# Optimization experiments

Hardware: AMD Instinct MI355X
Metric: run time of the kernel (lower is better)

Reference implementation:

```python
import jax, jax.numpy as jnp
import numpy as np
import math

B, N, K, C = 2, 8192, 16, 64
PE_DIM, HID = 32, 16
SIGMA, EPS = 1.0, 1e-06


def setup_inputs() -> dict:
    key = jax.random.key(0)
    ks = jax.random.split(key, 8)
    p = jax.random.normal(ks[0], (B, N, 3), jnp.float32)
    f = jax.random.normal(ks[1], (B, C, N), jnp.float32)
    pe = jax.random.normal(ks[2], (B, C, N, K), jnp.float32)
    knn_idx = jax.random.randint(ks[3], (B, N, K), 0, N, jnp.int32)
    # LocalAggregation convs1: 1x1 conv [C -> C] (+ReLU)
    W1 = jax.random.normal(ks[4], (C, C), jnp.float32) * (1.0 / math.sqrt(C))
    b1 = jnp.zeros((C,), jnp.float32)
    # GaussianKDEOffsetGenerator params: pe_mlp Linear(3->32), ffn Linear(32->16)->Linear(16->3)
    Wpe = jax.random.normal(ks[5], (PE_DIM, 3), jnp.float32) * (1.0 / math.sqrt(3))
    bpe = jnp.zeros((PE_DIM,), jnp.float32)
    Wh1 = jax.random.normal(ks[6], (HID, PE_DIM), jnp.float32) * (1.0 / math.sqrt(PE_DIM))
    bh1 = jnp.zeros((HID,), jnp.float32)
    Wh2 = jax.random.normal(ks[7], (3, HID), jnp.float32) * (1.0 / math.sqrt(HID))
    bh2 = jnp.zeros((3,), jnp.float32)
    return {"p": p, "f": f, "pe": pe, "W1": W1, "b1": b1, "Wpe": Wpe,
            "bpe": bpe, "Wh1": Wh1, "bh1": bh1, "Wh2": Wh2, "bh2": bh2,
            "knn_idx": knn_idx}


def reference(p, f, pe, W1, b1, Wpe, bpe, Wh1, bh1, Wh2, bh2, knn_idx):
    gather = jax.vmap(lambda a, i: a[i])  # per-batch neighbor gather
    # --- LocalAggregation: convs1 (1x1 conv + relu), group_by_idx, pe+fj, max-pool over K ---
    h = jax.nn.relu(jnp.einsum('oc,bcn->bon', W1, f) + b1[None, :, None])  # [B,C,N]
    ht = jnp.transpose(h, (0, 2, 1))                                       # [B,N,C]
    fj = gather(ht, knn_idx)                                               # [B,N,K,C]
    fout = jnp.max(pe + jnp.transpose(fj, (0, 3, 1, 2)), axis=-1)          # [B,C,N]
    # --- GaussianKDEOffsetGenerator on grouped neighbor coords [B*N, K, 3] ---
    coords = gather(p, knn_idx).reshape(B * N, K, 3)
    rel = coords[:, :, None, :] - coords[:, None, :, :]                    # [BN,K,K,3]
    pek = jax.nn.relu(jnp.einsum('nijc,dc->nijd', rel, Wpe) + bpe).mean(axis=2)  # [BN,K,PE]
    dist2 = jnp.sum(rel * rel, axis=-1)                                    # [BN,K,K]
    coef = 1.0 / math.sqrt(2.0 * math.pi * SIGMA ** 2 + EPS)
    kde = (coef * jnp.exp(-dist2 / (2.0 * SIGMA ** 2 + EPS))).sum(axis=2, keepdims=True)
    kde = kde / (jnp.max(kde, axis=1, keepdims=True) + EPS)                # [BN,K,1]
    fused = pek * kde
    delta = jax.nn.relu(fused @ Wh1.T + bh1) @ Wh2.T + bh2                 # [BN,K,3]
    return (fout, delta)
```

## Files before the change

### kernel.cpp

```cpp
#include <hip/hip_runtime.h>

#define B_ 2
#define N_ 8192
#define K_ 16
#define C_ 64
#define PE_ 32
#define HID_ 16

typedef float f4 __attribute__((ext_vector_type(4)));

__device__ __forceinline__ f4 splat4(float x) { f4 r = {x, x, x, x}; return r; }
__device__ __forceinline__ f4 relu4(f4 v) {
  f4 r;
  r[0] = fmaxf(v[0], 0.f); r[1] = fmaxf(v[1], 0.f);
  r[2] = fmaxf(v[2], 0.f); r[3] = fmaxf(v[3], 0.f);
  return r;
}
__device__ __forceinline__ float dot4(float4 w, f4 v) {
  return fmaf(w.x, v[0], fmaf(w.y, v[1], fmaf(w.z, v[2], w.w * v[3])));
}

struct PK4 { f4 k0, k1, k2, k3; };

__device__ __forceinline__ PK4 channel(const float4* __restrict__ sq,
                                       int d, const float* __restrict__ Wpe,
                                       const float* __restrict__ bpe) {
  const float wx = Wpe[d * 3 + 0], wy = Wpe[d * 3 + 1], wz = Wpe[d * 3 + 2];
  const float wb = bpe[d];
  const float4 A0 = sq[0], B0 = sq[1], C0 = sq[2];
  const float4 A1 = sq[3], B1 = sq[4], C1 = sq[5];
  const float4 A2 = sq[6], B2 = sq[7], C2 = sq[8];
  const float4 A3 = sq[9], B3 = sq[10], C3 = sq[11];
  const float p0  = fmaf(wx, A0.x, fmaf(wy, A0.y, wz * A0.z));
  const float p1  = fmaf(wx, A0.w, fmaf(wy, B0.x, wz * B0.y));
  const float p2  = fmaf(wx, B0.z, fmaf(wy, B0.w, wz * C0.x));
  const float p3  = fmaf(wx, C0.y, fmaf(wy, C0.z, wz * C0.w));
  const float p4  = fmaf(wx, A1.x, fmaf(wy, A1.y, wz * A1.z));
  const float p5  = fmaf(wx, A1.w, fmaf(wy, B1.x, wz * B1.y));
  const float p6  = fmaf(wx, B1.z, fmaf(wy, B1.w, wz * C1.x));
  const float p7  = fmaf(wx, C1.y, fmaf(wy, C1.z, wz * C1.w));
  const float p8  = fmaf(wx, A2.x, fmaf(wy, A2.y, wz * A2.z));
  const float p9  = fmaf(wx, A2.w, fmaf(wy, B2.x, wz * B2.y));
  const float p10 = fmaf(wx, B2.z, fmaf(wy, B2.w, wz * C2.x));
  const float p11 = fmaf(wx, C2.y, fmaf(wy, C2.z, wz * C2.w));
  const float p12 = fmaf(wx, A3.x, fmaf(wy, A3.y, wz * A3.z));
  const float p13 = fmaf(wx, A3.w, fmaf(wy, B3.x, wz * B3.y));
  const float p14 = fmaf(wx, B3.z, fmaf(wy, B3.w, wz * C3.x));
  const float p15 = fmaf(wx, C3.y, fmaf(wy, C3.z, wz * C3.w));
  const f4 a0 = {p0 + wb, p1 + wb, p2 + wb, p3 + wb};
  const f4 a1 = {p4 + wb, p5 + wb, p6 + wb, p7 + wb};
  const f4 a2 = {p8 + wb, p9 + wb, p10 + wb, p11 + wb};
  const f4 a3 = {p12 + wb, p13 + wb, p14 + wb, p15 + wb};
  f4 k0 = splat4(0.f), k1 = splat4(0.f), k2 = splat4(0.f), k3 = splat4(0.f);
#define KSTEP(PJ)                                  \
  {                                                \
    const f4 sp = splat4(PJ);                      \
    k0 += relu4(a0 - sp); k1 += relu4(a1 - sp);    \
    k2 += relu4(a2 - sp); k3 += relu4(a3 - sp);    \
  }
  KSTEP(p0) KSTEP(p1) KSTEP(p2) KSTEP(p3) KSTEP(p4) KSTEP(p5) KSTEP(p6)
  KSTEP(p7) KSTEP(p8) KSTEP(p9) KSTEP(p10) KSTEP(p11) KSTEP(p12) KSTEP(p13)
  KSTEP(p14) KSTEP(p15)
#undef KSTEP
  PK4 r; r.k0 = k0; r.k1 = k1; r.k2 = k2; r.k3 = k3;
  return r;
}

__global__ __launch_bounds__(256) void k1_conv(
    const float* __restrict__ f, const float* __restrict__ W1,
    const float* __restrict__ b1, float* __restrict__ ht) {
  const int t = threadIdx.x;
  const int lane = t & 63;
  const int w = t >> 6;
  const int g0 = blockIdx.x * 16 + w * 4;
  const int b = g0 >> 13;
  const int n = g0 & (N_ - 1);
  const f4* wp = reinterpret_cast<const f4*>(W1 + lane * C_);
  const f4 w0 = wp[0], w1 = wp[1], w2 = wp[2], w3 = wp[3];
  const f4 w4 = wp[4], w5 = wp[5], w6 = wp[6], w7 = wp[7];
  const f4 w8 = wp[8], w9 = wp[9], w10 = wp[10], w11 = wp[11];
  const f4 w12 = wp[12], w13 = wp[13], w14 = wp[14], w15 = wp[15];
  const float* fb = f + (size_t)b * C_ * N_ + n;
  f4 a = splat4(0.f);
#define CSTEP(Q, E)                                                        \
  {                                                                        \
    const f4 fv = *reinterpret_cast<const f4*>(fb + (size_t)(Q * 4 + E) * N_); \
    a += splat4(w##Q[E]) * fv;                                             \
  }
#define CQ(Q) CSTEP(Q, 0) CSTEP(Q, 1) CSTEP(Q, 2) CSTEP(Q, 3)
  CQ(0) CQ(1) CQ(2) CQ(3) CQ(4) CQ(5) CQ(6) CQ(7)
  CQ(8) CQ(9) CQ(10) CQ(11) CQ(12) CQ(13) CQ(14) CQ(15)
#undef CQ
#undef CSTEP
  const float bias = b1[lane];
  #pragma unroll
  for (int pt = 0; pt < 4; ++pt)
    ht[(size_t)(b * N_ + n + pt) * C_ + lane] = fmaxf(a[pt] + bias, 0.f);
}

#define GRPB 8
__global__ __launch_bounds__(256) void k23(
    const float* __restrict__ p, const float* __restrict__ pe,
    const float* __restrict__ ht, const int* __restrict__ knn,
    const float* __restrict__ Wpe, const float* __restrict__ bpe,
    const float* __restrict__ Wh1, const float* __restrict__ bh1,
    const float* __restrict__ Wh2, const float* __restrict__ bh2,
    float* __restrict__ fout, float* __restrict__ delta) {
  __shared__ __align__(16) char smem[19200];
  float* spk = (float*)smem;
  float* sc = (float*)(smem + 16384);
  float* sout = (float*)(smem + 16384);
  const int t = threadIdx.x;
  const int base = blockIdx.x * GRPB;
  const int b = base >> 13;
  const int n0b = base & (N_ - 1);
  const int g = t >> 5;
  const int l = t & 31;

  if (l < 16) {
    const int gid = base + g;
    const int idx = knn[(size_t)gid * K_ + l];
    const float* pp = p + (size_t)(b * N_ + idx) * 3;
    sc[g * 48 + l * 3 + 0] = pp[0];
    sc[g * 48 + l * 3 + 1] = pp[1];
    sc[g * 48 + l * 3 + 2] = pp[2];
  }
  __syncthreads();

  {
    const int d = l;
    const float4* sq = reinterpret_cast<const float4*>(&sc[g * 48]);
    const PK4 ck = channel(sq, d, Wpe, bpe);
    const int qw = d >> 2, pos = d & 3;
    float* gbase = spk + g * 512;
#define PKW(II, KV) \
    gbase[(II) * 32 + (((qw ^ ((II) & 7)) << 2) | pos)] = ck.KV[(II) & 3];
    PKW(0, k0) PKW(1, k0) PKW(2, k0) PKW(3, k0)
    PKW(4, k1) PKW(5, k1) PKW(6, k1) PKW(7, k1)
    PKW(8, k2) PKW(9, k2) PKW(10, k2) PKW(11, k2)
    PKW(12, k3) PKW(13, k3) PKW(14, k3) PKW(15, k3)
#undef PKW
  }
  __syncthreads();

  {
    const int i = t & 15, half = (t >> 4) & 1;
    const int gid = base + g;
    const float ci0 = sc[g * 48 + i * 3 + 0];
    const float ci1 = sc[g * 48 + i * 3 + 1];
    const float ci2 = sc[g * 48 + i * 3 + 2];
    const float4* sq = reinterpret_cast<const float4*>(&sc[g * 48]);
    const float INV2S = 0.49999975f;
    const float COEF = 0.39894225f;
    float kacc = 0.f;
    #pragma unroll
    for (int jj = 0; jj < 2; ++jj) {
      const int j4 = half * 2 + jj;
      const float4 a = sq[j4 * 3 + 0], b4 = sq[j4 * 3 + 1], c4 = sq[j4 * 3 + 2];
      float dx, dy, dz;
      dx = ci0 - a.x;  dy = ci1 - a.y;  dz = ci2 - a.z;
      kacc += __expf(-(dx * dx + dy * dy + dz * dz) * INV2S);
      dx = ci0 - a.w;  dy = ci1 - b4.x; dz = ci2 - b4.y;
      kacc += __expf(-(dx * dx + dy * dy + dz * dz) * INV2S);
      dx = ci0 - b4.z; dy = ci1 - b4.w; dz = ci2 - c4.x;
      kacc += __expf(-(dx * dx + dy * dy + dz * dz) * INV2S);
      dx = ci0 - c4.y; dy = ci1 - c4.z; dz = ci2 - c4.w;
      kacc += __expf(-(dx * dx + dy * dy + dz * dz) * INV2S);
    }
    kacc += __shfl_xor(kacc, 16);
    const float kde = COEF * kacc;
    float m = kde;
    m = fmaxf(m, __shfl_xor(m, 1));
    m = fmaxf(m, __shfl_xor(m, 2));
    m = fmaxf(m, __shfl_xor(m, 4));
    m = fmaxf(m, __shfl_xor(m, 8));
    const float s = (kde / (m + 1e-6f)) * (1.f / 16.f);

    const float* rbase = spk + g * 512 + i * 32;
    const int ix = i & 7;
    const f4 v0 = *reinterpret_cast<const f4*>(&rbase[(0 ^ ix) << 2]);
    const f4 v1 = *reinterpret_cast<const f4*>(&rbase[(1 ^ ix) << 2]);
    const f4 v2 = *reinterpret_cast<const f4*>(&rbase[(2 ^ ix) << 2]);
    const f4 v3 = *reinterpret_cast<const f4*>(&rbase[(3 ^ ix) << 2]);
    const f4 v4 = *reinterpret_cast<const f4*>(&rbase[(4 ^ ix) << 2]);
    const f4 v5 = *reinterpret_cast<const f4*>(&rbase[(5 ^ ix) << 2]);
    const f4 v6 = *reinterpret_cast<const f4*>(&rbase[(6 ^ ix) << 2]);
    const f4 v7 = *reinterpret_cast<const f4*>(&rbase[(7 ^ ix) << 2]);

    float o0 = 0.f, o1 = 0.f, o2 = 0.f;
    #pragma unroll
    for (int hh = 0; hh < 8; ++hh) {
      const int h = half * 8 + hh;
      const float4* Wr = reinterpret_cast<const float4*>(Wh1 + h * PE_);
      const float u = dot4(Wr[0], v0) + dot4(Wr[1], v1) + dot4(Wr[2], v2) +
                      dot4(Wr[3], v3) + dot4(Wr[4], v4) + dot4(Wr[5], v5) +
                      dot4(Wr[6], v6) + dot4(Wr[7], v7);
      const float a = fmaxf(fmaf(s, u, bh1[h]), 0.f);
      o0 = fmaf(Wh2[0 * HID_ + h], a, o0);
      o1 = fmaf(Wh2[1 * HID_ + h], a, o1);
      o2 = fmaf(Wh2[2 * HID_ + h], a, o2);
    }
    o0 += __shfl_xor(o0, 16);
    o1 += __shfl_xor(o1, 16);
    o2 += __shfl_xor(o2, 16);
    if (half == 0) {
      float* dp = delta + ((size_t)gid * K_ + i) * 3;
      dp[0] = o0 + bh2[0];
      dp[1] = o1 + bh2[1];
      dp[2] = o2 + bh2[2];
    }
  }
  __syncthreads();

  {
    const int lane = t & 63;
    const int w = t >> 6;
    #pragma unroll
    for (int pp2 = 0; pp2 < 2; ++pp2) {
      const int npt = w * 2 + pp2;
      const int gid = base + npt;
      const int* kn = knn + (size_t)gid * K_;
      const f4* per = reinterpret_cast<const f4*>(
          pe + ((size_t)(b * C_ + lane) * N_ + n0b + npt) * K_);
      const f4 q0 = per[0], q1 = per[1], q2 = per[2], q3 = per[3];
      float mx = -3.402823466e+38f;
#define PVK(KK, QV)                                                       \
      {                                                                   \
        const int id = kn[KK];                                            \
        const float hv = ht[(size_t)(b * N_ + id) * C_ + lane];           \
        mx = fmaxf(mx, QV[(KK) & 3] + hv);                                \
      }
      PVK(0, q0) PVK(1, q0) PVK(2, q0) PVK(3, q0)
      PVK(4, q1) PVK(5, q1) PVK(6, q1) PVK(7, q1)
      PVK(8, q2) PVK(9, q2) PVK(10, q2) PVK(11, q2)
      PVK(12, q3) PVK(13, q3) PVK(14, q3) PVK(15, q3)
#undef PVK
      sout[lane * 11 + npt] = mx;
    }
    __syncthreads();
    const int c = t >> 2, nq = (t & 3) * 2;
    float2 r = make_float2(sout[c * 11 + nq], sout[c * 11 + nq + 1]);
    *reinterpret_cast<float2*>(fout + (size_t)(b * C_ + c) * N_ + n0b + nq) = r;
  }
}

extern "C" void kernel_launch(void* const* d_in, const int* in_sizes, int n_in,
                              void* d_out, int out_size, void* d_ws, size_t ws_size,
                              hipStream_t stream) {
  const float* p   = (const float*)d_in[0];
  const float* f   = (const float*)d_in[1];
  const float* pe  = (const float*)d_in[2];
  const float* W1  = (const float*)d_in[3];
  const float* b1  = (const float*)d_in[4];
  const float* Wpe = (const float*)d_in[5];
  const float* bpe = (const float*)d_in[6];
  const float* Wh1 = (const float*)d_in[7];
  const float* bh1 = (const float*)d_in[8];
  const float* Wh2 = (const float*)d_in[9];
  const float* bh2 = (const float*)d_in[10];
  const int* knn   = (const int*)d_in[11];
  float* fout  = (float*)d_out;
  float* delta = (float*)d_out + (size_t)B_ * C_ * N_;
  float* ht = (float*)d_ws;

  k1_conv<<<(B_ * N_) / 16, 256, 0, stream>>>(f, W1, b1, ht);
  k23<<<(B_ * N_) / GRPB, 256, 0, stream>>>(p, pe, ht, knn, Wpe, bpe, Wh1, bh1,
                                            Wh2, bh2, fout, delta);
}
```

Measured before the change: 66.35 us.

## Split aggregation from KDE kernel and coalesce pe loads via LDS slab

Moves the neighbor max-pool aggregation out of the fused KDE kernel into its own kernel, k2_agg. Each wave stages the gathered ht rows in an LDS slab, so that each lane then reads 16-byte pe chunks that sit contiguously across neighbors. The old version read four f4 per lane with a per-channel stride. pe is read with nontemporal loads, and the max over K is finished with lane shuffles. This adds an extra kernel launch and gives up the overlap between the two workloads, in exchange for better-coalesced streaming of the large pe tensor and lower LDS use in the KDE kernel.

```diff
diff --git a/kernel.cpp b/kernel.cpp
--- a/kernel.cpp
+++ b/kernel.cpp
@@ -98,22 +98,60 @@
     ht[(size_t)(b * N_ + n + pt) * C_ + lane] = fmaxf(a[pt] + bias, 0.f);
 }
 
+#define SLAB 20
+__global__ __launch_bounds__(256) void k2_agg(
+    const float* __restrict__ pe, const float* __restrict__ ht,
+    const int* __restrict__ knn, float* __restrict__ fout) {
+  __shared__ float slab[4][C_ * SLAB];
+  const int t = threadIdx.x;
+  const int wv = t >> 6;
+  const int lane = t & 63;
+  float* my = &slab[wv][0];
+  const int base = blockIdx.x * 8 + wv * 2;
+  const int b = base >> 13;
+  const int n0 = base & (N_ - 1);
+  const int c16 = lane >> 2;
+  const int k4 = lane & 3;
+
+  #pragma unroll
+  for (int pt = 0; pt < 2; ++pt) {
+    const int n = n0 + pt;
+    const int* kn = knn + (size_t)(b * N_ + n) * K_;
+    #pragma unroll
+    for (int k = 0; k < K_; ++k) {
+      const int id = kn[k];
+      my[lane * SLAB + k] = ht[(size_t)(b * N_ + id) * C_ + lane];
+    }
+    #pragma unroll
+    for (int it = 0; it < 4; ++it) {
+      const int c = it * 16 + c16;
+      const f4 pv = __builtin_nontemporal_load(reinterpret_cast<const f4*>(
+          pe + ((size_t)(b * C_ + c) * N_ + n) * K_ + k4 * 4));
+      const f4 fj = *reinterpret_cast<const f4*>(&my[c * SLAB + k4 * 4]);
+      float v = fmaxf(fmaxf(pv[0] + fj[0], pv[1] + fj[1]),
+                      fmaxf(pv[2] + fj[2], pv[3] + fj[3]));
+      v = fmaxf(v, __shfl_xor(v, 1));
+      v = fmaxf(v, __shfl_xor(v, 2));
+      if (k4 == 0) my[c * SLAB + 16 + pt] = v;
+    }
+  }
+  const float2 r = make_float2(my[lane * SLAB + 16], my[lane * SLAB + 17]);
+  *reinterpret_cast<float2*>(fout + (size_t)(b * C_ + lane) * N_ + n0) = r;
+}
+
 #define GRPB 8
-__global__ __launch_bounds__(256) void k23(
-    const float* __restrict__ p, const float* __restrict__ pe,
-    const float* __restrict__ ht, const int* __restrict__ knn,
+__global__ __launch_bounds__(256) void k3_kde(
+    const float* __restrict__ p, const int* __restrict__ knn,
     const float* __restrict__ Wpe, const float* __restrict__ bpe,
     const float* __restrict__ Wh1, const float* __restrict__ bh1,
     const float* __restrict__ Wh2, const float* __restrict__ bh2,
-    float* __restrict__ fout, float* __restrict__ delta) {
-  __shared__ __align__(16) char smem[19200];
+    float* __restrict__ delta) {
+  __shared__ __align__(16) char smem[17920];
   float* spk = (float*)smem;
   float* sc = (float*)(smem + 16384);
-  float* sout = (float*)(smem + 16384);
   const int t = threadIdx.x;
   const int base = blockIdx.x * GRPB;
   const int b = base >> 13;
-  const int n0b = base & (N_ - 1);
   const int g = t >> 5;
   const int l = t & 31;
 
@@ -209,38 +247,6 @@
       dp[1] = o1 + bh2[1];
       dp[2] = o2 + bh2[2];
     }
-  }
-  __syncthreads();
-
-  {
-    const int lane = t & 63;
-    const int w = t >> 6;
-    #pragma unroll
-    for (int pp2 = 0; pp2 < 2; ++pp2) {
-      const int npt = w * 2 + pp2;
-      const int gid = base + npt;
-      const int* kn = knn + (size_t)gid * K_;
-      const f4* per = reinterpret_cast<const f4*>(
-          pe + ((size_t)(b * C_ + lane) * N_ + n0b + npt) * K_);
-      const f4 q0 = per[0], q1 = per[1], q2 = per[2], q3 = per[3];
-      float mx = -3.402823466e+38f;
-#define PVK(KK, QV)                                                       \
-      {                                                                   \
-        const int id = kn[KK];                                            \
-        const float hv = ht[(size_t)(b * N_ + id) * C_ + lane];           \
-        mx = fmaxf(mx, QV[(KK) & 3] + hv);                                \
-      }
-      PVK(0, q0) PVK(1, q0) PVK(2, q0) PVK(3, q0)
-      PVK(4, q1) PVK(5, q1) PVK(6, q1) PVK(7, q1)
-      PVK(8, q2) PVK(9, q2) PVK(10, q2) PVK(11, q2)
-      PVK(12, q3) PVK(13, q3) PVK(14, q3) PVK(15, q3)
-#undef PVK
-      sout[lane * 11 + npt] = mx;
-    }
-    __syncthreads();
-    const int c = t >> 2, nq = (t & 3) * 2;
-    float2 r = make_float2(sout[c * 11 + nq], sout[c * 11 + nq + 1]);
-    *reinterpret_cast<float2*>(fout + (size_t)(b * C_ + c) * N_ + n0b + nq) = r;
   }
 }
 
@@ -264,6 +270,7 @@
   float* ht = (float*)d_ws;
 
   k1_conv<<<(B_ * N_) / 16, 256, 0, stream>>>(f, W1, b1, ht);
-  k23<<<(B_ * N_) / GRPB, 256, 0, stream>>>(p, pe, ht, knn, Wpe, bpe, Wh1, bh1,
-                                            Wh2, bh2, fout, delta);
-}
+  k2_agg<<<(B_ * N_) / 8, 256, 0, stream>>>(pe, ht, knn, fout);
+  k3_kde<<<(B_ * N_) / GRPB, 256, 0, stream>>>(p, knn, Wpe, bpe, Wh1, bh1,
+                                               Wh2, bh2, delta);
+}
```

Measured after the change: 83.42 us. 1.26x slower.

## Split fused kernel into separate max-pool and KDE block roles with coalesced pe loads

Applied to the files above, without the earlier changes.

The fused kernel becomes a launch with two block roles. The first 1024 blocks handle the neighbor max-pool for 16 points each: they stage gathered ht rows in padded shared memory, then read pe with contiguous nontemporal vector loads and reduce the max with shuffles. The remaining blocks run the KDE/offset MLP as before. This targets the strided per-channel pe access of the old layout and lets the bandwidth-bound and compute-bound roles overlap across the GPU. The cost is extra shared-memory traffic and more barriers in the pooling blocks.

```diff
diff --git a/kernel.cpp b/kernel.cpp
--- a/kernel.cpp
+++ b/kernel.cpp
@@ -98,149 +98,164 @@
     ht[(size_t)(b * N_ + n + pt) * C_ + lane] = fmaxf(a[pt] + bias, 0.f);
 }
 
-#define GRPB 8
-__global__ __launch_bounds__(256) void k23(
+#define SFJ_STRIDE 65
+#define SOUT_OFF 16640
+#define NP2 1024
+__global__ __launch_bounds__(256) void k23_split(
     const float* __restrict__ p, const float* __restrict__ pe,
     const float* __restrict__ ht, const int* __restrict__ knn,
     const float* __restrict__ Wpe, const float* __restrict__ bpe,
     const float* __restrict__ Wh1, const float* __restrict__ bh1,
     const float* __restrict__ Wh2, const float* __restrict__ bh2,
     float* __restrict__ fout, float* __restrict__ delta) {
-  __shared__ __align__(16) char smem[19200];
-  float* spk = (float*)smem;
-  float* sc = (float*)(smem + 16384);
-  float* sout = (float*)(smem + 16384);
+  __shared__ __align__(16) char smem[21760];
   const int t = threadIdx.x;
-  const int base = blockIdx.x * GRPB;
-  const int b = base >> 13;
-  const int n0b = base & (N_ - 1);
-  const int g = t >> 5;
-  const int l = t & 31;
-
-  if (l < 16) {
-    const int gid = base + g;
-    const int idx = knn[(size_t)gid * K_ + l];
-    const float* pp = p + (size_t)(b * N_ + idx) * 3;
-    sc[g * 48 + l * 3 + 0] = pp[0];
-    sc[g * 48 + l * 3 + 1] = pp[1];
-    sc[g * 48 + l * 3 + 2] = pp[2];
-  }
-  __syncthreads();
-
-  {
-    const int d = l;
-    const float4* sq = reinterpret_cast<const float4*>(&sc[g * 48]);
-    const PK4 ck = channel(sq, d, Wpe, bpe);
-    const int qw = d >> 2, pos = d & 3;
-    float* gbase = spk + g * 512;
-#define PKW(II, KV) \
-    gbase[(II) * 32 + (((qw ^ ((II) & 7)) << 2) | pos)] = ck.KV[(II) & 3];
-    PKW(0, k0) PKW(1, k0) PKW(2, k0) PKW(3, k0)
-    PKW(4, k1) PKW(5, k1) PKW(6, k1) PKW(7, k1)
-    PKW(8, k2) PKW(9, k2) PKW(10, k2) PKW(11, k2)
-    PKW(12, k3) PKW(13, k3) PKW(14, k3) PKW(15, k3)
-#undef PKW
-  }
-  __syncthreads();
-
-  {
-    const int i = t & 15, half = (t >> 4) & 1;
-    const int gid = base + g;
-    const float ci0 = sc[g * 48 + i * 3 + 0];
-    const float ci1 = sc[g * 48 + i * 3 + 1];
-    const float ci2 = sc[g * 48 + i * 3 + 2];
-    const float4* sq = reinterpret_cast<const float4*>(&sc[g * 48]);
-    const float INV2S = 0.49999975f;
-    const float COEF = 0.39894225f;
-    float kacc = 0.f;
-    #pragma unroll
-    for (int jj = 0; jj < 2; ++jj) {
-      const int j4 = half * 2 + jj;
-      const float4 a = sq[j4 * 3 + 0], b4 = sq[j4 * 3 + 1], c4 = sq[j4 * 3 + 2];
-      float dx, dy, dz;
-      dx = ci0 - a.x;  dy = ci1 - a.y;  dz = ci2 - a.z;
-      kacc += __expf(-(dx * dx + dy * dy + dz * dz) * INV2S);
-      dx = ci0 - a.w;  dy = ci1 - b4.x; dz = ci2 - b4.y;
-      kacc += __expf(-(dx * dx + dy * dy + dz * dz) * INV2S);
-      dx = ci0 - b4.z; dy = ci1 - b4.w; dz = ci2 - c4.x;
-      kacc += __expf(-(dx * dx + dy * dy + dz * dz) * INV2S);
-      dx = ci0 - c4.y; dy = ci1 - c4.z; dz = ci2 - c4.w;
-      kacc += __expf(-(dx * dx + dy * dy + dz * dz) * INV2S);
-    }
-    kacc += __shfl_xor(kacc, 16);
-    const float kde = COEF * kacc;
-    float m = kde;
-    m = fmaxf(m, __shfl_xor(m, 1));
-    m = fmaxf(m, __shfl_xor(m, 2));
-    m = fmaxf(m, __shfl_xor(m, 4));
-    m = fmaxf(m, __shfl_xor(m, 8));
-    const float s = (kde / (m + 1e-6f)) * (1.f / 16.f);
-
-    const float* rbase = spk + g * 512 + i * 32;
-    const int ix = i & 7;
-    const f4 v0 = *reinterpret_cast<const f4*>(&rbase[(0 ^ ix) << 2]);
-    const f4 v1 = *reinterpret_cast<const f4*>(&rbase[(1 ^ ix) << 2]);
-    const f4 v2 = *reinterpret_cast<const f4*>(&rbase[(2 ^ ix) << 2]);
-    const f4 v3 = *reinterpret_cast<const f4*>(&rbase[(3 ^ ix) << 2]);
-    const f4 v4 = *reinterpret_cast<const f4*>(&rbase[(4 ^ ix) << 2]);
-    const f4 v5 = *reinterpret_cast<const f4*>(&rbase[(5 ^ ix) << 2]);
-    const f4 v6 = *reinterpret_cast<const f4*>(&rbase[(6 ^ ix) << 2]);
-    const f4 v7 = *reinterpret_cast<const f4*>(&rbase[(7 ^ ix) << 2]);
-
-    float o0 = 0.f, o1 = 0.f, o2 = 0.f;
-    #pragma unroll
-    for (int hh = 0; hh < 8; ++hh) {
-      const int h = half * 8 + hh;
-      const float4* Wr = reinterpret_cast<const float4*>(Wh1 + h * PE_);
-      const float u = dot4(Wr[0], v0) + dot4(Wr[1], v1) + dot4(Wr[2], v2) +
-                      dot4(Wr[3], v3) + dot4(Wr[4], v4) + dot4(Wr[5], v5) +
-                      dot4(Wr[6], v6) + dot4(Wr[7], v7);
-      const float a = fmaxf(fmaf(s, u, bh1[h]), 0.f);
-      o0 = fmaf(Wh2[0 * HID_ + h], a, o0);
-      o1 = fmaf(Wh2[1 * HID_ + h], a, o1);
-      o2 = fmaf(Wh2[2 * HID_ + h], a, o2);
-    }
-    o0 += __shfl_xor(o0, 16);
-    o1 += __shfl_xor(o1, 16);
-    o2 += __shfl_xor(o2, 16);
-    if (half == 0) {
-      float* dp = delta + ((size_t)gid * K_ + i) * 3;
-      dp[0] = o0 + bh2[0];
-      dp[1] = o1 + bh2[1];
-      dp[2] = o2 + bh2[2];
-    }
-  }
-  __syncthreads();
-
-  {
+
+  if (blockIdx.x < NP2) {
+    float* sfj = (float*)smem;
+    float* sout = (float*)(smem + SOUT_OFF);
+    const int base = blockIdx.x * 16;
+    const int b = base >> 13;
+    const int n0b = base & (N_ - 1);
     const int lane = t & 63;
     const int w = t >> 6;
-    #pragma unroll
-    for (int pp2 = 0; pp2 < 2; ++pp2) {
-      const int npt = w * 2 + pp2;
-      const int gid = base + npt;
-      const int* kn = knn + (size_t)gid * K_;
-      const f4* per = reinterpret_cast<const f4*>(
-          pe + ((size_t)(b * C_ + lane) * N_ + n0b + npt) * K_);
-      const f4 q0 = per[0], q1 = per[1], q2 = per[2], q3 = per[3];
-      float mx = -3.402823466e+38f;
-#define PVK(KK, QV)                                                       \
-      {                                                                   \
-        const int id = kn[KK];                                            \
-        const float hv = ht[(size_t)(b * N_ + id) * C_ + lane];           \
-        mx = fmaxf(mx, QV[(KK) & 3] + hv);                                \
-      }
-      PVK(0, q0) PVK(1, q0) PVK(2, q0) PVK(3, q0)
-      PVK(4, q1) PVK(5, q1) PVK(6, q1) PVK(7, q1)
-      PVK(8, q2) PVK(9, q2) PVK(10, q2) PVK(11, q2)
-      PVK(12, q3) PVK(13, q3) PVK(14, q3) PVK(15, q3)
-#undef PVK
-      sout[lane * 11 + npt] = mx;
+    const int csub = lane >> 4, sl = lane & 15;
+    const int j = sl & 3, nn = sl >> 2;
+    #pragma unroll 1
+    for (int si = 0; si < 4; ++si) {
+      const int n0 = n0b + si * 4;
+      #pragma unroll
+      for (int n = 0; n < 4; ++n) {
+        const int* kn = knn + (size_t)(b * N_ + n0 + n) * K_ + w * 4;
+        #pragma unroll
+        for (int kk = 0; kk < 4; ++kk) {
+          const int id = kn[kk];
+          const float hv = ht[(size_t)(b * N_ + id) * C_ + lane];
+          sfj[lane * SFJ_STRIDE + (n * 4 + w) * 4 + kk] = hv;
+        }
+      }
+      __syncthreads();
+      #pragma unroll
+      for (int it2 = 0; it2 < 4; ++it2) {
+        const int c = it2 * 16 + w * 4 + csub;
+        const f4 pv = __builtin_nontemporal_load(
+            reinterpret_cast<const f4*>(pe + ((size_t)(b * C_ + c) * N_ + n0) * K_) + sl);
+        const f4 fj = *reinterpret_cast<const f4*>(&sfj[c * SFJ_STRIDE + sl * 4]);
+        float v = fmaxf(fmaxf(pv[0] + fj[0], pv[1] + fj[1]),
+                        fmaxf(pv[2] + fj[2], pv[3] + fj[3]));
+        v = fmaxf(v, __shfl_xor(v, 1));
+        v = fmaxf(v, __shfl_xor(v, 2));
+        if (j == 0) sout[c * 20 + si * 4 + nn] = v;
+      }
+      __syncthreads();
+    }
+    const int c = t >> 2, q = t & 3;
+    const float4 r = *reinterpret_cast<const float4*>(&sout[c * 20 + q * 4]);
+    *reinterpret_cast<float4*>(fout + (size_t)(b * C_ + c) * N_ + n0b + q * 4) = r;
+    return;
+  }
+
+  {
+    float* spk = (float*)smem;
+    float* sc = (float*)(smem + 16384);
+    const int base = (blockIdx.x - NP2) * 8;
+    const int b = base >> 13;
+    const int g = t >> 5;
+    const int l = t & 31;
+
+    if (l < 16) {
+      const int gid = base + g;
+      const int idx = knn[(size_t)gid * K_ + l];
+      const float* pp = p + (size_t)(b * N_ + idx) * 3;
+      sc[g * 48 + l * 3 + 0] = pp[0];
+      sc[g * 48 + l * 3 + 1] = pp[1];
+      sc[g * 48 + l * 3 + 2] = pp[2];
     }
     __syncthreads();
-    const int c = t >> 2, nq = (t & 3) * 2;
-    float2 r = make_float2(sout[c * 11 + nq], sout[c * 11 + nq + 1]);
-    *reinterpret_cast<float2*>(fout + (size_t)(b * C_ + c) * N_ + n0b + nq) = r;
+
+    {
+      const int d = l;
+      const float4* sq = reinterpret_cast<const float4*>(&sc[g * 48]);
+      const PK4 ck = channel(sq, d, Wpe, bpe);
+      const int qw = d >> 2, pos = d & 3;
+      float* gbase = spk + g * 512;
+#define PKW(II, KV) \
+      gbase[(II) * 32 + (((qw ^ ((II) & 7)) << 2) | pos)] = ck.KV[(II) & 3];
+      PKW(0, k0) PKW(1, k0) PKW(2, k0) PKW(3, k0)
+      PKW(4, k1) PKW(5, k1) PKW(6, k1) PKW(7, k1)
+      PKW(8, k2) PKW(9, k2) PKW(10, k2) PKW(11, k2)
+      PKW(12, k3) PKW(13, k3) PKW(14, k3) PKW(15, k3)
+#undef PKW
+    }
+    __syncthreads();
+
+    {
+      const int i = t & 15, half = (t >> 4) & 1;
+      const int gid = base + g;
+      const float ci0 = sc[g * 48 + i * 3 + 0];
+      const float ci1 = sc[g * 48 + i * 3 + 1];
+      const float ci2 = sc[g * 48 + i * 3 + 2];
+      const float4* sq = reinterpret_cast<const float4*>(&sc[g * 48]);
+      const float INV2S = 0.49999975f;
+      const float COEF = 0.39894225f;
+      float kacc = 0.f;
+      #pragma unroll
+      for (int jj = 0; jj < 2; ++jj) {
+        const int j4 = half * 2 + jj;
+        const float4 a = sq[j4 * 3 + 0], b4 = sq[j4 * 3 + 1], c4 = sq[j4 * 3 + 2];
+        float dx, dy, dz;
+        dx = ci0 - a.x;  dy = ci1 - a.y;  dz = ci2 - a.z;
+        kacc += __expf(-(dx * dx + dy * dy + dz * dz) * INV2S);
+        dx = ci0 - a.w;  dy = ci1 - b4.x; dz = ci2 - b4.y;
+        kacc += __expf(-(dx * dx + dy * dy + dz * dz) * INV2S);
+        dx = ci0 - b4.z; dy = ci1 - b4.w; dz = ci2 - c4.x;
+        kacc += __expf(-(dx * dx + dy * dy + dz * dz) * INV2S);
+        dx = ci0 - c4.y; dy = ci1 - c4.z; dz = ci2 - c4.w;
+        kacc += __expf(-(dx * dx + dy * dy + dz * dz) * INV2S);
+      }
+      kacc += __shfl_xor(kacc, 16);
+      const float kde = COEF * kacc;
+      float m = kde;
+      m = fmaxf(m, __shfl_xor(m, 1));
+      m = fmaxf(m, __shfl_xor(m, 2));
+      m = fmaxf(m, __shfl_xor(m, 4));
+      m = fmaxf(m, __shfl_xor(m, 8));
+      const float s = (kde / (m + 1e-6f)) * (1.f / 16.f);
+
+      const float* rbase = spk + g * 512 + i * 32;
+      const int ix = i & 7;
+      const f4 v0 = *reinterpret_cast<const f4*>(&rbase[(0 ^ ix) << 2]);
+      const f4 v1 = *reinterpret_cast<const f4*>(&rbase[(1 ^ ix) << 2]);
+      const f4 v2 = *reinterpret_cast<const f4*>(&rbase[(2 ^ ix) << 2]);
+      const f4 v3 = *reinterpret_cast<const f4*>(&rbase[(3 ^ ix) << 2]);
+      const f4 v4 = *reinterpret_cast<const f4*>(&rbase[(4 ^ ix) << 2]);
+      const f4 v5 = *reinterpret_cast<const f4*>(&rbase[(5 ^ ix) << 2]);
+      const f4 v6 = *reinterpret_cast<const f4*>(&rbase[(6 ^ ix) << 2]);
+      const f4 v7 = *reinterpret_cast<const f4*>(&rbase[(7 ^ ix) << 2]);
+
+      float o0 = 0.f, o1 = 0.f, o2 = 0.f;
+      #pragma unroll
+      for (int hh = 0; hh < 8; ++hh) {
+        const int h = half * 8 + hh;
+        const float4* Wr = reinterpret_cast<const float4*>(Wh1 + h * PE_);
+        const float u = dot4(Wr[0], v0) + dot4(Wr[1], v1) + dot4(Wr[2], v2) +
+                        dot4(Wr[3], v3) + dot4(Wr[4], v4) + dot4(Wr[5], v5) +
+                        dot4(Wr[6], v6) + dot4(Wr[7], v7);
+        const float a = fmaxf(fmaf(s, u, bh1[h]), 0.f);
+        o0 = fmaf(Wh2[0 * HID_ + h], a, o0);
+        o1 = fmaf(Wh2[1 * HID_ + h], a, o1);
+        o2 = fmaf(Wh2[2 * HID_ + h], a, o2);
+      }
+      o0 += __shfl_xor(o0, 16);
+      o1 += __shfl_xor(o1, 16);
+      o2 += __shfl_xor(o2, 16);
+      if (half == 0) {
+        float* dp = delta + ((size_t)gid * K_ + i) * 3;
+        dp[0] = o0 + bh2[0];
+        dp[1] = o1 + bh2[1];
+        dp[2] = o2 + bh2[2];
+      }
+    }
   }
 }
 
@@ -264,6 +279,6 @@
   float* ht = (float*)d_ws;
 
   k1_conv<<<(B_ * N_) / 16, 256, 0, stream>>>(f, W1, b1, ht);
-  k23<<<(B_ * N_) / GRPB, 256, 0, stream>>>(p, pe, ht, knn, Wpe, bpe, Wh1, bh1,
-                                            Wh2, bh2, fout, delta);
-}
+  k23_split<<<NP2 + (B_ * N_) / 8, 256, 0, stream>>>(
+      p, pe, ht, knn, Wpe, bpe, Wh1, bh1, Wh2, bh2, fout, delta);
+}
```

Result: no change. 65.99 us (-0.5%).
